# Optimization experiments

Hardware: AMD Instinct MI355X
Metric: run time of the kernel (lower is better)

## Reference

```python
import jax, jax.numpy as jnp
import numpy as np

N = 8192
DIN = 128
DOUT = 128
EPS = 1e-7
GAMMA_MAX = 1e7


def _mobius_scalar_mul(r, x):
    # Moebius scalar multiplication on the Poincare ball (c=1):
    # r (.) x = tanh(r * arctanh(||x||)) * x / ||x||
    n = jnp.linalg.norm(x, axis=-1, keepdims=True)
    n_safe = jnp.clip(n, EPS, 1.0 - EPS)
    return jnp.tanh(r * jnp.arctanh(n_safe)) * x / n_safe


def _logmap0(x):
    n = jnp.linalg.norm(x, axis=-1, keepdims=True)
    n_safe = jnp.clip(n, EPS, 1.0 - EPS)
    return jnp.arctanh(n_safe) * x / n_safe


def _expmap0(v):
    n = jnp.linalg.norm(v, axis=-1, keepdims=True)
    n_safe = jnp.maximum(n, EPS)
    return jnp.tanh(n_safe) * v / n_safe


def setup_inputs() -> dict:
    key = jax.random.key(0)
    k1, k2, k3, k4 = jax.random.split(key, 4)
    # node features inside the Poincare ball (small norm)
    x = 0.01 * jax.random.normal(k1, (N, DIN), dtype=jnp.float32)
    # sparse-ish binary adjacency stored dense (module treats adj as dense [N,N])
    adj = (jax.random.uniform(k2, (N, N)) < 0.004).astype(jnp.float32)
    W = 0.05 * jax.random.normal(k3, (DIN, DOUT), dtype=jnp.float32)
    b = 0.05 * jax.random.normal(k4, (DOUT,), dtype=jnp.float32)
    return {"x": x, "adj": adj, "W": W, "b": b}


def reference(x, adj, W, b):
    n = adj.shape[0]
    # adj <- I + adj, then symmetric degree normalization D^{-1/2} A D^{-1/2}
    a = jnp.eye(n, dtype=adj.dtype) + adj
    D = 1.0 / jnp.sqrt(jnp.sum(a, axis=1))
    a = a * D[:, None] * D[None, :]
    # gyromidpoint-style weighted aggregation (gamma broadcast over rows, as in torch)
    r2 = jnp.sum(x * x, axis=-1, keepdims=True)            # [N,1]
    gamma = jnp.minimum(2.0 / (1.0 - r2), GAMMA_MAX)        # [N,1]
    num = a * gamma                                          # [N,N]
    den = jnp.sum(a * (gamma - 1.0), axis=-1, keepdims=True)  # [N,1]
    coef = num / den                                         # [N,N]
    aggr = coef @ x                                          # [N,DIN]
    aggr = _mobius_scalar_mul(0.5, aggr)
    # PoincareFC: logmap0 -> linear -> act -> expmap0 (to_tan=False)
    u = _logmap0(aggr)
    y = jax.nn.relu(u @ W + b)
    return _expmap0(y)
```

## Files before the change

kernel.cpp:

```cpp
#include <hip/hip_runtime.h>
#include <cstdint>
#include <cstddef>

#define N_NODES 8192
#define DIN 128
#define CAP 128
#define EPSF 1e-7f
#define RPB 4

typedef unsigned short u16;

__global__ __launch_bounds__(256) void k_build(const float4* __restrict__ adj,
                                               u16* __restrict__ cols,
                                               int* __restrict__ counts,
                                               float* __restrict__ Dv) {
    const int lane = threadIdx.x & 63;
    const int row  = blockIdx.x * 4 + (threadIdx.x >> 6);
    const float4* rp = adj + (size_t)row * (N_NODES / 4);
    u16* cl = cols + (size_t)row * CAP;
    const unsigned long long lt_mask = (1ULL << lane) - 1ULL;

    int base = 0;
#pragma unroll 2
    for (int it = 0; it < N_NODES / 256; ++it) {
        float4 v = rp[it * 64 + lane];
        int cb = it * 256 + lane * 4;
        {
            bool nz = (v.x != 0.0f);
            unsigned long long m = __ballot(nz);
            if (nz) { int p = base + __popcll(m & lt_mask); if (p < CAP) cl[p] = (u16)(cb + 0); }
            base += __popcll(m);
        }
        {
            bool nz = (v.y != 0.0f);
            unsigned long long m = __ballot(nz);
            if (nz) { int p = base + __popcll(m & lt_mask); if (p < CAP) cl[p] = (u16)(cb + 1); }
            base += __popcll(m);
        }
        {
            bool nz = (v.z != 0.0f);
            unsigned long long m = __ballot(nz);
            if (nz) { int p = base + __popcll(m & lt_mask); if (p < CAP) cl[p] = (u16)(cb + 2); }
            base += __popcll(m);
        }
        {
            bool nz = (v.w != 0.0f);
            unsigned long long m = __ballot(nz);
            if (nz) { int p = base + __popcll(m & lt_mask); if (p < CAP) cl[p] = (u16)(cb + 3); }
            base += __popcll(m);
        }
    }
    if (lane == 0) {
        counts[row] = base;
        Dv[row] = 1.0f / sqrtf(1.0f + (float)base);
    }
}

__device__ __forceinline__ float blockSum128(float v, volatile float* red, int tid) {
#pragma unroll
    for (int m = 32; m >= 1; m >>= 1) v += __shfl_xor(v, m, 64);
    __syncthreads();
    if ((tid & 63) == 0) red[tid >> 6] = v;
    __syncthreads();
    return red[0] + red[1];
}

__global__ __launch_bounds__(128) void k_fused(const float* __restrict__ x,
                                               const float* __restrict__ Dv,
                                               const u16* __restrict__ cols,
                                               const int* __restrict__ counts,
                                               const float* __restrict__ W,
                                               const float* __restrict__ b,
                                               float* __restrict__ out) {
    __shared__ u16   colsL[CAP];
    __shared__ float djL[CAP];
    __shared__ float red[2];
    __shared__ float uL[RPB][DIN];

    const int d    = threadIdx.x;
    const int row0 = blockIdx.x * RPB;

    for (int r = 0; r < RPB; ++r) {
        const int row = row0 + r;
        int c = counts[row];
        if (c > CAP) c = CAP;
        colsL[d] = cols[(size_t)row * CAP + d];
        const float xi = x[(size_t)row * DIN + d];
        const float Di = Dv[row];
        djL[d] = (d < c) ? Dv[colsL[d]] : 0.0f;
        __syncthreads();

        float acc  = Di * xi;
        float sumw = Di;
#pragma unroll 4
        for (int k = 0; k < c; ++k) {
            int   j  = colsL[k];
            float dj = djL[k];
            sumw += dj;
            acc = fmaf(dj, x[(size_t)j * DIN + d], acc);
        }

        float r2 = blockSum128(xi * xi, red, d);
        float gamma = fminf(2.0f / (1.0f - r2), 1e7f);
        float ag = (gamma / ((gamma - 1.0f) * sumw)) * acc;

        float n2 = blockSum128(ag * ag, red, d);
        float n  = sqrtf(n2);
        float nsafe = fminf(fmaxf(n, EPSF), 1.0f - EPSF);
        float t  = tanhf(0.5f * atanhf(nsafe));
        float nm = t * (n / nsafe);
        float nmsafe = fminf(fmaxf(nm, EPSF), 1.0f - EPSF);
        uL[r][d] = (atanhf(nmsafe) / nmsafe) * (t / nsafe) * ag;
    }
    __syncthreads();

    float av[RPB];
#pragma unroll
    for (int r = 0; r < RPB; ++r) av[r] = b[d];
    const float* Wc = W + d;
#pragma unroll 4
    for (int k = 0; k < DIN; ++k) {
        float wkd = Wc[(size_t)k * DIN];
#pragma unroll
        for (int r = 0; r < RPB; ++r)
            av[r] = fmaf(uL[r][k], wkd, av[r]);
    }

#pragma unroll
    for (int r = 0; r < RPB; ++r) {
        float y  = fmaxf(av[r], 0.0f);
        float ss = blockSum128(y * y, red, d);
        float ny = sqrtf(ss);
        float ns = fmaxf(ny, EPSF);
        float sc = tanhf(ns) / ns;
        out[(size_t)(row0 + r) * DIN + d] = y * sc;
    }
}

extern "C" void kernel_launch(void* const* d_in, const int* in_sizes, int n_in,
                              void* d_out, int out_size, void* d_ws, size_t ws_size,
                              hipStream_t stream) {
    const float* x   = (const float*)d_in[0];
    const float* adj = (const float*)d_in[1];
    const float* W   = (const float*)d_in[2];
    const float* b   = (const float*)d_in[3];
    float* out = (float*)d_out;

    char* ws = (char*)d_ws;
    int*   counts = (int*)ws;
    float* Dv     = (float*)(ws + 32768);
    u16*   cols   = (u16*)(ws + 65536);

    hipLaunchKernelGGL(k_build, dim3(N_NODES / 4), dim3(256), 0, stream,
                       (const float4*)adj, cols, counts, Dv);
    hipLaunchKernelGGL(k_fused, dim3(N_NODES / RPB), dim3(128), 0, stream,
                       x, Dv, cols, counts, W, b, out);
}
```

Baseline: 403.5 us.

## Assign one wavefront per row in fused kernel and stream adjacency with nontemporal loads

The fused aggregation kernel now processes four rows in parallel, one 64-lane wavefront per row with float2 loads, instead of looping over rows with a 128-thread block. This removes block-wide barrier reductions in favour of wave shuffles and raises parallelism. The build kernel reads the dense adjacency with nontemporal loads and a deeper unroll so the 256 MB stream does not pollute cache. The linear layer is split so each half of the block computes two output rows. The build kernel, which streams the full adjacency, probably dominates runtime, so the overall effect is bounded.

```diff
diff --git a/kernel.cpp b/kernel.cpp
--- a/kernel.cpp
+++ b/kernel.cpp
@@ -6,24 +6,25 @@
 #define DIN 128
 #define CAP 128
 #define EPSF 1e-7f
-#define RPB 4
 
 typedef unsigned short u16;
+typedef unsigned int u32;
+typedef float nfloat4 __attribute__((ext_vector_type(4)));
 
-__global__ __launch_bounds__(256) void k_build(const float4* __restrict__ adj,
+__global__ __launch_bounds__(256) void k_build(const nfloat4* __restrict__ adj,
                                                u16* __restrict__ cols,
                                                int* __restrict__ counts,
                                                float* __restrict__ Dv) {
     const int lane = threadIdx.x & 63;
     const int row  = blockIdx.x * 4 + (threadIdx.x >> 6);
-    const float4* rp = adj + (size_t)row * (N_NODES / 4);
+    const nfloat4* rp = adj + (size_t)row * (N_NODES / 4);
     u16* cl = cols + (size_t)row * CAP;
     const unsigned long long lt_mask = (1ULL << lane) - 1ULL;
 
     int base = 0;
-#pragma unroll 2
+#pragma unroll 4
     for (int it = 0; it < N_NODES / 256; ++it) {
-        float4 v = rp[it * 64 + lane];
+        nfloat4 v = __builtin_nontemporal_load(&rp[it * 64 + lane]);
         int cb = it * 256 + lane * 4;
         {
             bool nz = (v.x != 0.0f);
@@ -56,85 +57,99 @@
     }
 }
 
-__device__ __forceinline__ float blockSum128(float v, volatile float* red, int tid) {
+__device__ __forceinline__ float waveSum(float v) {
 #pragma unroll
     for (int m = 32; m >= 1; m >>= 1) v += __shfl_xor(v, m, 64);
-    __syncthreads();
-    if ((tid & 63) == 0) red[tid >> 6] = v;
-    __syncthreads();
-    return red[0] + red[1];
+    return v;
 }
 
-__global__ __launch_bounds__(128) void k_fused(const float* __restrict__ x,
+__global__ __launch_bounds__(256) void k_fused(const float* __restrict__ x,
                                                const float* __restrict__ Dv,
                                                const u16* __restrict__ cols,
                                                const int* __restrict__ counts,
                                                const float* __restrict__ W,
                                                const float* __restrict__ b,
                                                float* __restrict__ out) {
-    __shared__ u16   colsL[CAP];
-    __shared__ float djL[CAP];
-    __shared__ float red[2];
-    __shared__ float uL[RPB][DIN];
+    __shared__ u16   colsL[4][CAP];
+    __shared__ float djL[4][CAP];
+    __shared__ float uL[4][DIN];
+    __shared__ float red[8];
 
-    const int d    = threadIdx.x;
-    const int row0 = blockIdx.x * RPB;
+    const int tid = threadIdx.x;
+    const int w   = tid >> 6;
+    const int l   = tid & 63;
+    const int row0 = blockIdx.x * 4;
+    const int row  = row0 + w;
+    const float2* x2 = (const float2*)x;
 
-    for (int r = 0; r < RPB; ++r) {
-        const int row = row0 + r;
-        int c = counts[row];
-        if (c > CAP) c = CAP;
-        colsL[d] = cols[(size_t)row * CAP + d];
-        const float xi = x[(size_t)row * DIN + d];
-        const float Di = Dv[row];
-        djL[d] = (d < c) ? Dv[colsL[d]] : 0.0f;
-        __syncthreads();
+    int c = counts[row];
+    if (c > CAP) c = CAP;
 
-        float acc  = Di * xi;
-        float sumw = Di;
+    ((u32*)colsL[w])[l] = ((const u32*)(cols + (size_t)row * CAP))[l];
+    {
+        int k0 = 2 * l, k1 = 2 * l + 1;
+        int j0 = colsL[w][k0], j1 = colsL[w][k1];
+        djL[w][k0] = (k0 < c) ? Dv[j0] : 0.0f;
+        djL[w][k1] = (k1 < c) ? Dv[j1] : 0.0f;
+    }
+    const float2 xi = x2[(size_t)row * 64 + l];
+    const float  Di = Dv[row];
+
+    float ax = Di * xi.x, ay = Di * xi.y;
+    float sumw = Di;
 #pragma unroll 4
-        for (int k = 0; k < c; ++k) {
-            int   j  = colsL[k];
-            float dj = djL[k];
-            sumw += dj;
-            acc = fmaf(dj, x[(size_t)j * DIN + d], acc);
-        }
+    for (int k = 0; k < c; ++k) {
+        int   j  = colsL[w][k];
+        float dj = djL[w][k];
+        sumw += dj;
+        float2 xj = x2[(size_t)j * 64 + l];
+        ax = fmaf(dj, xj.x, ax);
+        ay = fmaf(dj, xj.y, ay);
+    }
 
-        float r2 = blockSum128(xi * xi, red, d);
-        float gamma = fminf(2.0f / (1.0f - r2), 1e7f);
-        float ag = (gamma / ((gamma - 1.0f) * sumw)) * acc;
+    float r2 = waveSum(fmaf(xi.x, xi.x, xi.y * xi.y));
+    float gamma = fminf(2.0f / (1.0f - r2), 1e7f);
+    float s = gamma / ((gamma - 1.0f) * sumw);
+    ax *= s; ay *= s;
 
-        float n2 = blockSum128(ag * ag, red, d);
-        float n  = sqrtf(n2);
-        float nsafe = fminf(fmaxf(n, EPSF), 1.0f - EPSF);
-        float t  = tanhf(0.5f * atanhf(nsafe));
-        float nm = t * (n / nsafe);
-        float nmsafe = fminf(fmaxf(nm, EPSF), 1.0f - EPSF);
-        uL[r][d] = (atanhf(nmsafe) / nmsafe) * (t / nsafe) * ag;
-    }
+    float n2 = waveSum(fmaf(ax, ax, ay * ay));
+    float n  = sqrtf(n2);
+    float nsafe = fminf(fmaxf(n, EPSF), 1.0f - EPSF);
+    float t  = tanhf(0.5f * atanhf(nsafe));
+    float nm = t * (n / nsafe);
+    float nmsafe = fminf(fmaxf(nm, EPSF), 1.0f - EPSF);
+    float us = (atanhf(nmsafe) / nmsafe) * (t / nsafe);
+    ((float2*)uL[w])[l] = make_float2(us * ax, us * ay);
+
     __syncthreads();
 
-    float av[RPB];
-#pragma unroll
-    for (int r = 0; r < RPB; ++r) av[r] = b[d];
+    const int h = tid >> 7;
+    const int d = tid & 127;
+    const float bd = b[d];
+    float a0 = bd, a1 = bd;
     const float* Wc = W + d;
-#pragma unroll 4
+    const float* u0 = uL[2 * h];
+    const float* u1 = uL[2 * h + 1];
+#pragma unroll 8
     for (int k = 0; k < DIN; ++k) {
         float wkd = Wc[(size_t)k * DIN];
-#pragma unroll
-        for (int r = 0; r < RPB; ++r)
-            av[r] = fmaf(uL[r][k], wkd, av[r]);
+        a0 = fmaf(u0[k], wkd, a0);
+        a1 = fmaf(u1[k], wkd, a1);
     }
 
-#pragma unroll
-    for (int r = 0; r < RPB; ++r) {
-        float y  = fmaxf(av[r], 0.0f);
-        float ss = blockSum128(y * y, red, d);
-        float ny = sqrtf(ss);
-        float ns = fmaxf(ny, EPSF);
-        float sc = tanhf(ns) / ns;
-        out[(size_t)(row0 + r) * DIN + d] = y * sc;
-    }
+    float y0 = fmaxf(a0, 0.0f), y1 = fmaxf(a1, 0.0f);
+    float s0 = waveSum(y0 * y0);
+    float s1 = waveSum(y1 * y1);
+    if (l == 0) { red[w * 2] = s0; red[w * 2 + 1] = s1; }
+    __syncthreads();
+    float ss0 = red[4 * h + 0] + red[4 * h + 2];
+    float ss1 = red[4 * h + 1] + red[4 * h + 3];
+    float ns0 = fmaxf(sqrtf(ss0), EPSF);
+    float ns1 = fmaxf(sqrtf(ss1), EPSF);
+    float sc0 = tanhf(ns0) / ns0;
+    float sc1 = tanhf(ns1) / ns1;
+    out[(size_t)(row0 + 2 * h) * DIN + d]     = y0 * sc0;
+    out[(size_t)(row0 + 2 * h + 1) * DIN + d] = y1 * sc1;
 }
 
 extern "C" void kernel_launch(void* const* d_in, const int* in_sizes, int n_in,
@@ -152,7 +167,7 @@
     u16*   cols   = (u16*)(ws + 65536);
 
     hipLaunchKernelGGL(k_build, dim3(N_NODES / 4), dim3(256), 0, stream,
-                       (const float4*)adj, cols, counts, Dv);
-    hipLaunchKernelGGL(k_fused, dim3(N_NODES / RPB), dim3(128), 0, stream,
+                       (const nfloat4*)adj, cols, counts, Dv);
+    hipLaunchKernelGGL(k_fused, dim3(N_NODES / 4), dim3(256), 0, stream,
                        x, Dv, cols, counts, W, b, out);
 }
```

Measured after the change: 373.1 us. 1.08x faster.
